# Kernel tuning notes

Hardware: AMD Instinct MI355X
Metric: run time of the kernel (lower is better)

The kernel has to match this reference:

```python
import jax, jax.numpy as jnp
import numpy as np

B, T, DKQ, DV, EKQ, EV, H, OUT = 8, 2048, 64, 64, 128, 128, 4, 32
FF = 4 * EV
NEG = -1e30  # additive mask value (safe stand-in for -inf)


def _ln(x, g, b, eps=1e-5):
    m = x.mean(-1, keepdims=True)
    var = ((x - m) ** 2).mean(-1, keepdims=True)
    return (x - m) * jax.lax.rsqrt(var + eps) * g + b


def _attn(q, k, v, mask):
    # q,k,v: [n, T, E] -> heads [n, H, T, dh]; NOTE: no 1/sqrt(d) scaling (faithful to source)
    n, t, _ = q.shape
    q = q.reshape(n, t, H, -1).transpose(0, 2, 1, 3)
    k = k.reshape(n, t, H, -1).transpose(0, 2, 1, 3)
    v = v.reshape(n, t, H, -1).transpose(0, 2, 1, 3)
    w = jnp.einsum('bhqd,bhkd->bhqk', q, k) + mask  # [n,H,T,T]
    a = jax.nn.softmax(w, axis=-1)
    o = jnp.einsum('bhqk,bhkd->bhqd', a, v)
    return o.transpose(0, 2, 1, 3).reshape(n, t, -1)


def setup_inputs() -> dict:
    key = jax.random.key(0)
    ks = jax.random.split(key, 32)
    w = lambda k, s: jax.random.normal(k, s, jnp.float32) * 0.02
    DIN_A = DKQ + DV
    return {
        'kq': jax.random.normal(ks[0], (B, T, DKQ), jnp.float32),
        'v': jax.random.normal(ks[1], (B, T, DV), jnp.float32),
        # Layer A (input_dim = DKQ+DV, embed = EV)
        'A_Wk': w(ks[2], (DIN_A, EV)), 'A_bk': jnp.zeros((EV,), jnp.float32),
        'A_Wq': w(ks[3], (DIN_A, EV)), 'A_bq': jnp.zeros((EV,), jnp.float32),
        'A_Wv': w(ks[4], (DIN_A, EV)), 'A_bv': jnp.zeros((EV,), jnp.float32),
        'A_f1W': w(ks[5], (EV, FF)), 'A_f1b': jnp.zeros((FF,), jnp.float32),
        'A_f2W': w(ks[6], (FF, EV)), 'A_f2b': jnp.zeros((EV,), jnp.float32),
        'A_n1g': jnp.ones((EV,), jnp.float32), 'A_n1b': jnp.zeros((EV,), jnp.float32),
        'A_n2g': jnp.ones((EV,), jnp.float32), 'A_n2b': jnp.zeros((EV,), jnp.float32),
        # Layer B (kq -> EKQ, vA -> EV)
        'B_Wk': w(ks[7], (DKQ, EKQ)), 'B_bk': jnp.zeros((EKQ,), jnp.float32),
        'B_Wq': w(ks[8], (DKQ, EKQ)), 'B_bq': jnp.zeros((EKQ,), jnp.float32),
        'B_Wv': w(ks[9], (EV, EV)), 'B_bv': jnp.zeros((EV,), jnp.float32),
        'B_f1W': w(ks[10], (EV, FF)), 'B_f1b': jnp.zeros((FF,), jnp.float32),
        'B_f2W': w(ks[11], (FF, EV)), 'B_f2b': jnp.zeros((EV,), jnp.float32),
        # Output head
        'out_W': w(ks[12], (EV, OUT)), 'out_b': jnp.zeros((OUT,), jnp.float32),
    }


def reference(kq, v, A_Wk, A_bk, A_Wq, A_bq, A_Wv, A_bv, A_f1W, A_f1b, A_f2W, A_f2b,
              A_n1g, A_n1b, A_n2g, A_n2b, B_Wk, B_bk, B_Wq, B_bq, B_Wv, B_bv,
              B_f1W, B_f1b, B_f2W, B_f2b, out_W, out_b):
    n, t, _ = kq.shape
    i = jnp.arange(t)[:, None]
    j = jnp.arange(t)[None, :]
    mask_a = jnp.where(j <= i, 0.0, NEG).astype(jnp.float32)               # causal (diag=1)
    mask_b = jnp.where((j < i) | ((i == 0) & (j == 0)), 0.0, NEG).astype(jnp.float32)  # strict causal + (0,0) exception

    # ---- Layer A ----
    X = jnp.concatenate([kq, v], axis=-1)
    K = X @ A_Wk + A_bk
    Q = X @ A_Wq + A_bq
    V = X @ A_Wv + A_bv
    attn_out = _attn(Q, K, V, mask_a)
    h1 = _ln(V + attn_out, A_n1g, A_n1b)
    ff = jax.nn.gelu(h1 @ A_f1W + A_f1b, approximate=False) @ A_f2W + A_f2b
    vA = _ln(h1 + ff, A_n2g, A_n2b)

    # ---- Layer B (no residuals / norms: values is overwritten in source) ----
    K2 = kq @ B_Wk + B_bk
    Q2 = kq @ B_Wq + B_bq
    V2 = vA @ B_Wv + B_bv
    attn_out2 = _attn(Q2, K2, V2, mask_b)
    ff2 = jax.nn.gelu(attn_out2 @ B_f1W + B_f1b, approximate=False) @ B_f2W + B_f2b

    return ff2 @ out_W + out_b
```

## Files before the change

### kernel.cpp

```cpp
#include <hip/hip_runtime.h>
#include <hip/hip_bf16.h>

#define TSEQ 2048
#define NBATCH 8
#define NROWS (NBATCH*TSEQ)
#define EMB 128
#define NH 4
#define DH 32
#define OUTD 32
#define APLANE (NROWS*EMB)

typedef short s8v __attribute__((ext_vector_type(8)));
typedef float f4v __attribute__((ext_vector_type(4)));

__device__ __forceinline__ unsigned short f2bf(float f){
  unsigned int u = __float_as_uint(f);
  unsigned int r = u + 0x7fffu + ((u >> 16) & 1u);
  return (unsigned short)(r >> 16);
}
__device__ __forceinline__ float bf2f(unsigned short u){
  return __uint_as_float(((unsigned int)u) << 16);
}

struct WPack {
  const float* src[10];
  int off[10];
  int ntk[10];
  int rowoff[10];
  int nsh[10];
  int kn[10];
};
__global__ __launch_bounds__(256) void prep_w(WPack p, short* __restrict__ warena){
  int blk = blockIdx.x, m = 0;
  #pragma unroll
  for (int i=0;i<10;i++){
    int nb = p.kn[i] >> 8;
    if (blk < nb){ m = i; break; }
    blk -= nb;
  }
  int idx = blk*256 + threadIdx.x;
  float x = p.src[m][idx];
  int nsh = p.nsh[m];
  int n = idx & ((1<<nsh)-1);
  int k = idx >> nsh;
  int K = p.kn[m] >> nsh;
  unsigned short hi = f2bf(x);
  unsigned short lo = f2bf(x - bf2f(hi));
  short* dh = warena + p.off[m] + (size_t)(p.rowoff[m] + n)*K + k;
  dh[0]        = (short)hi;
  dh[p.ntk[m]] = (short)lo;
}

__global__ __launch_bounds__(256) void xsplit(const float* __restrict__ kq, const float* __restrict__ v,
                                              unsigned short* __restrict__ X){
  int idx = blockIdx.x*256 + threadIdx.x;
  int row = idx >> 7, c = idx & 127;
  float val = (c < 64) ? kq[row*64 + c] : v[row*64 + (c-64)];
  unsigned short hi = f2bf(val);
  X[idx]          = hi;
  X[idx + APLANE] = f2bf(val - bf2f(hi));
}

struct GOuts {
  const float* bias[3];
  float* of[3];
  unsigned short* ob[3];
};
__global__ __launch_bounds__(256) void gemm2(
    const unsigned short* __restrict__ A, int aplane, int lda, int K, int niter,
    const short* __restrict__ wt, int NTK,
    GOuts og, int NT, int nseg, int act){
  __shared__ short As[2][2][64*40];
  const int tid  = threadIdx.x;
  const int w    = tid >> 6;
  const int lane = tid & 63;
  const int col  = lane & 15;
  const int quad = lane >> 4;
  const int row0 = blockIdx.x * 64;
  const int colg = blockIdx.y*64 + w*16 + col;
  const bool two = (aplane != 0);

  f4v acc[4];
  #pragma unroll
  for (int i=0;i<4;i++) acc[i] = (f4v){0.f,0.f,0.f,0.f};

  const int ar = tid >> 2, ac = (tid & 3)*8;
  const unsigned short* abase = A + (size_t)(row0 + ar)*lda;

  s8v pah, pal;
  pah = *(const s8v*)(abase + ac);
  if (two) pal = *(const s8v*)(abase + aplane + ac);

  for (int i=0;i<niter;i++){
    const int buf = i & 1;
    *(s8v*)&As[buf][0][ar*40 + ac] = pah;
    if (two) *(s8v*)&As[buf][1][ar*40 + ac] = pal;
    __syncthreads();
    if (i+1 < niter){
      const int kcol = (i+1)*32 + ac;
      pah = *(const s8v*)(abase + kcol);
      if (two) pal = *(const s8v*)(abase + aplane + kcol);
    }
    const short* wp = wt + (size_t)colg*K + i*32 + quad*8;
    s8v bh = *(const s8v*)wp;
    s8v bl = *(const s8v*)(wp + NTK);
    #pragma unroll
    for (int rt=0;rt<4;rt++){
      s8v ah = *(const s8v*)&As[buf][0][(rt*16 + col)*40 + quad*8];
      acc[rt] = __builtin_amdgcn_mfma_f32_16x16x32_bf16(ah, bh, acc[rt], 0, 0, 0);
      if (two){
        s8v al = *(const s8v*)&As[buf][1][(rt*16 + col)*40 + quad*8];
        acc[rt] = __builtin_amdgcn_mfma_f32_16x16x32_bf16(al, bh, acc[rt], 0, 0, 0);
      }
      acc[rt] = __builtin_amdgcn_mfma_f32_16x16x32_bf16(ah, bl, acc[rt], 0, 0, 0);
    }
  }

  int seg, lcol, ldc;
  if (nseg > 1){ seg = colg >> 7; lcol = colg & 127; ldc = 128; }
  else         { seg = 0; lcol = colg; ldc = NT; }
  const float bv = og.bias[seg][lcol];
  float* of = og.of[seg];
  unsigned short* ob = og.ob[seg];
  #pragma unroll
  for (int rt=0;rt<4;rt++){
    #pragma unroll
    for (int r=0;r<4;r++){
      const int row = row0 + rt*16 + quad*4 + r;
      float val = acc[rt][r] + bv;
      if (act == 1) val = 0.5f*val*(1.f + erff(val*0.70710678118654752440f));
      if (ob) ob[(size_t)row*ldc + lcol] = f2bf(val);
      else    of[(size_t)row*ldc + lcol] = val;
    }
  }
}

__global__ __launch_bounds__(256) void vtrans(const float* __restrict__ V, unsigned short* __restrict__ Vtb){
  __shared__ short Lt[64*40];
  const int tid = threadIdx.x;
  const int t0 = blockIdx.x * 64;
  const int bh = blockIdx.y;
  const int b = bh >> 2, h = bh & 3;
  {
    const int r = tid >> 2, c = (tid & 3)*8;
    const float* src = V + (size_t)(b*TSEQ + t0 + r)*EMB + h*DH + c;
    float4 x0 = *(const float4*)src;
    float4 x1 = *(const float4*)(src + 4);
    s8v kb;
    kb[0]=(short)f2bf(x0.x); kb[1]=(short)f2bf(x0.y); kb[2]=(short)f2bf(x0.z); kb[3]=(short)f2bf(x0.w);
    kb[4]=(short)f2bf(x1.x); kb[5]=(short)f2bf(x1.y); kb[6]=(short)f2bf(x1.z); kb[7]=(short)f2bf(x1.w);
    *(s8v*)&Lt[r*40 + c] = kb;
  }
  __syncthreads();
  const int d = tid >> 3, kc = (tid & 7)*8;
  s8v o;
  #pragma unroll
  for (int j=0;j<8;j++) o[j] = Lt[(kc + j)*40 + d];
  *(s8v*)(Vtb + ((size_t)bh*32 + d)*TSEQ + t0 + kc) = o;
}

#define KT_STRIDE 40
#define VT_STRIDE 72
#define PW_STRIDE 72
__global__ __launch_bounds__(128) void flash3(const unsigned short* __restrict__ Qb,
                                              const unsigned short* __restrict__ Kb,
                                              const unsigned short* __restrict__ Vtb,
                                              float* __restrict__ O0, float* __restrict__ O1,
                                              float* __restrict__ L0, float* __restrict__ L1,
                                              int mode){
  __shared__ short Kt[64*KT_STRIDE];
  __shared__ short Vt[32*VT_STRIDE];
  __shared__ short Pw[2][16*PW_STRIDE];
  const int tid  = threadIdx.x;
  const int w    = tid >> 6;
  const int lane = tid & 63;
  const int col  = lane & 15;
  const int quad = lane >> 4;
  const int bh = blockIdx.y;
  const int b = bh >> 2, h = bh & 3;
  const int par = blockIdx.z;
  float* Op = par ? O1 : O0;
  float* Lp = par ? L1 : L0;
  const int kr = tid >> 1, kc16 = (tid & 1)*16;
  const int vd = tid >> 2, vk16 = (tid & 3)*16;

  for (int pass = 0; pass < 2; pass++){
    const int t = pass ? blockIdx.x : (63 - blockIdx.x);
    const int qbase = t*32 + w*16;
    const int jtmax = t >> 1;

    s8v qf = *(const s8v*)(Qb + (size_t)(b*TSEQ + qbase + col)*EMB + h*DH + quad*8);
    f4v o0 = {0.f,0.f,0.f,0.f}, o1 = {0.f,0.f,0.f,0.f};
    float lr[4] = {0.f,0.f,0.f,0.f};

    if (par <= jtmax){
      s8v ka, kb2, va, vb;
      {
        const unsigned short* kp = Kb + (size_t)(b*TSEQ + par*64 + kr)*EMB + h*DH + kc16;
        ka = *(const s8v*)kp; kb2 = *(const s8v*)(kp + 8);
        const unsigned short* vp = Vtb + ((size_t)bh*32 + vd)*TSEQ + par*64 + vk16;
        va = *(const s8v*)vp; vb = *(const s8v*)(vp + 8);
      }
      for (int jt = par; jt <= jtmax; jt += 2){
        __syncthreads();
        *(s8v*)&Kt[kr*KT_STRIDE + kc16]     = ka;
        *(s8v*)&Kt[kr*KT_STRIDE + kc16 + 8] = kb2;
        *(s8v*)&Vt[vd*VT_STRIDE + vk16]     = va;
        *(s8v*)&Vt[vd*VT_STRIDE + vk16 + 8] = vb;
        __syncthreads();
        if (jt + 2 <= jtmax){
          const unsigned short* kp = Kb + (size_t)(b*TSEQ + (jt+2)*64 + kr)*EMB + h*DH + kc16;
          ka = *(const s8v*)kp; kb2 = *(const s8v*)(kp + 8);
          const unsigned short* vp = Vtb + ((size_t)bh*32 + vd)*TSEQ + (jt+2)*64 + vk16;
          va = *(const s8v*)vp; vb = *(const s8v*)(vp + 8);
        }
        f4v s[4];
        #pragma unroll
        for (int t4=0;t4<4;t4++){
          s8v kf = *(const s8v*)&Kt[(t4*16 + col)*KT_STRIDE + quad*8];
          f4v z = {0.f,0.f,0.f,0.f};
          s[t4] = __builtin_amdgcn_mfma_f32_16x16x32_bf16(qf, kf, z, 0, 0, 0);
        }
        if (jt == jtmax){
          const int j0 = jt*64;
          #pragma unroll
          for (int t4=0;t4<4;t4++){
            const int jg = j0 + t4*16 + col;
            #pragma unroll
            for (int r=0;r<4;r++){
              const int qg = qbase + quad*4 + r;
              const bool ok = (mode==0) ? (jg <= qg) : ((jg < qg) || (qg==0 && jg==0));
              s[t4][r] = ok ? s[t4][r] : -1e30f;
            }
          }
        }
        #pragma unroll
        for (int t4=0;t4<4;t4++){
          #pragma unroll
          for (int r=0;r<4;r++){
            float pv = __expf(s[t4][r]);
            s[t4][r] = pv;
            lr[r] += pv;
            Pw[w][(quad*4+r)*PW_STRIDE + t4*16 + col] = (short)f2bf(pv);
          }
        }
        #pragma unroll
        for (int kk=0;kk<2;kk++){
          s8v pf  = *(const s8v*)&Pw[w][col*PW_STRIDE + kk*32 + quad*8];
          s8v vf0 = *(const s8v*)&Vt[(col)*VT_STRIDE    + kk*32 + quad*8];
          s8v vf1 = *(const s8v*)&Vt[(16+col)*VT_STRIDE + kk*32 + quad*8];
          o0 = __builtin_amdgcn_mfma_f32_16x16x32_bf16(pf, vf0, o0, 0, 0, 0);
          o1 = __builtin_amdgcn_mfma_f32_16x16x32_bf16(pf, vf1, o1, 0, 0, 0);
        }
      }
    }
    float* obase = Op + (size_t)(b*TSEQ + qbase)*EMB + h*DH;
    #pragma unroll
    for (int r=0;r<4;r++){
      float l = lr[r];
      l += __shfl_xor(l,1); l += __shfl_xor(l,2);
      l += __shfl_xor(l,4); l += __shfl_xor(l,8);
      obase[(size_t)(quad*4+r)*EMB + col]      = o0[r];
      obase[(size_t)(quad*4+r)*EMB + 16 + col] = o1[r];
      if (col == 0) Lp[(size_t)(b*TSEQ + qbase + quad*4 + r)*NH + h] = l;
    }
  }
}

__global__ __launch_bounds__(64) void combine_ln(const float* __restrict__ O0, const float* __restrict__ O1,
                                                 const float* __restrict__ L0, const float* __restrict__ L1,
                                                 const float* __restrict__ Vf,
                                                 const float* __restrict__ g, const float* __restrict__ bt,
                                                 unsigned short* __restrict__ outp){
  const int row = blockIdx.x;
  const int tid = threadIdx.x;
  const size_t base = (size_t)row*EMB;
  const int h0 = tid >> 5, h1i = 2 + (tid >> 5);
  const float la = L0[(size_t)row*NH + h0] + L1[(size_t)row*NH + h0];
  const float lb = L0[(size_t)row*NH + h1i] + L1[(size_t)row*NH + h1i];
  float x0 = Vf[base+tid]    + (O0[base+tid]    + O1[base+tid])    / la;
  float x1 = Vf[base+tid+64] + (O0[base+tid+64] + O1[base+tid+64]) / lb;
  float s  = x0 + x1;
  float s2 = x0*x0 + x1*x1;
  #pragma unroll
  for (int off=1; off<64; off<<=1){
    s  += __shfl_xor(s,  off);
    s2 += __shfl_xor(s2, off);
  }
  float mean = s * (1.f/128.f);
  float var  = s2 * (1.f/128.f) - mean*mean;
  float rstd = rsqrtf(var + 1e-5f);
  float y0 = (x0-mean)*rstd*g[tid]    + bt[tid];
  float y1 = (x1-mean)*rstd*g[tid+64] + bt[tid+64];
  unsigned short h0b = f2bf(y0), h1b = f2bf(y1);
  outp[base+tid]             = h0b;
  outp[base+tid+64]          = h1b;
  outp[base+tid+APLANE]      = f2bf(y0 - bf2f(h0b));
  outp[base+tid+64+APLANE]   = f2bf(y1 - bf2f(h1b));
}

__global__ __launch_bounds__(64) void ln2(const unsigned short* __restrict__ Xp, const float* __restrict__ R,
                                          const float* __restrict__ g, const float* __restrict__ bt,
                                          unsigned short* __restrict__ outp){
  const int row = blockIdx.x;
  const int tid = threadIdx.x;
  const size_t base = (size_t)row*EMB;
  float x0 = bf2f(Xp[base+tid])    + bf2f(Xp[base+tid+APLANE])    + R[base+tid];
  float x1 = bf2f(Xp[base+tid+64]) + bf2f(Xp[base+tid+64+APLANE]) + R[base+tid+64];
  float s  = x0 + x1;
  float s2 = x0*x0 + x1*x1;
  #pragma unroll
  for (int off=1; off<64; off<<=1){
    s  += __shfl_xor(s,  off);
    s2 += __shfl_xor(s2, off);
  }
  float mean = s * (1.f/128.f);
  float var  = s2 * (1.f/128.f) - mean*mean;
  float rstd = rsqrtf(var + 1e-5f);
  float y0 = (x0-mean)*rstd*g[tid]    + bt[tid];
  float y1 = (x1-mean)*rstd*g[tid+64] + bt[tid+64];
  unsigned short h0b = f2bf(y0), h1b = f2bf(y1);
  outp[base+tid]             = h0b;
  outp[base+tid+64]          = h1b;
  outp[base+tid+APLANE]      = f2bf(y0 - bf2f(h0b));
  outp[base+tid+64+APLANE]   = f2bf(y1 - bf2f(h1b));
}

__global__ __launch_bounds__(256) void combine_b(const float* __restrict__ O0, const float* __restrict__ O1,
                                                 const float* __restrict__ L0, const float* __restrict__ L1,
                                                 unsigned short* __restrict__ outp){
  const int idx = blockIdx.x*256 + threadIdx.x;
  const int row = idx >> 7, c = idx & 127, h = c >> 5;
  const float l = L0[(size_t)row*NH + h] + L1[(size_t)row*NH + h];
  const float v = (O0[idx] + O1[idx]) / l;
  unsigned short hb = f2bf(v);
  outp[idx]          = hb;
  outp[idx + APLANE] = f2bf(v - bf2f(hb));
}

__global__ __launch_bounds__(256) void out_proj(const float* __restrict__ A,
                                                const float* __restrict__ W, const float* __restrict__ bb,
                                                float* __restrict__ out){
  __shared__ float As[8*128];
  __shared__ float Ws2[128*32];
  const int tid = threadIdx.x;
  const int row0 = blockIdx.x * 8;
  for (int idx = tid; idx < 8*128; idx += 256) As[idx] = A[(size_t)row0*128 + idx];
  for (int idx = tid; idx < 128*32; idx += 256) Ws2[idx] = W[idx];
  __syncthreads();
  const int r = tid >> 5, c = tid & 31;
  float acc = bb[c];
  #pragma unroll 8
  for (int k=0;k<128;k++) acc = fmaf(As[r*128 + k], Ws2[k*32 + c], acc);
  out[(size_t)(row0 + r)*OUTD + c] = acc;
}

extern "C" void kernel_launch(void* const* d_in, const int* in_sizes, int n_in,
                              void* d_out, int out_size, void* d_ws, size_t ws_size,
                              hipStream_t stream) {
  const float* kq    = (const float*)d_in[0];
  const float* v     = (const float*)d_in[1];
  const float* A_Wk  = (const float*)d_in[2];  const float* A_bk  = (const float*)d_in[3];
  const float* A_Wq  = (const float*)d_in[4];  const float* A_bq  = (const float*)d_in[5];
  const float* A_Wv  = (const float*)d_in[6];  const float* A_bv  = (const float*)d_in[7];
  const float* A_f1W = (const float*)d_in[8];  const float* A_f1b = (const float*)d_in[9];
  const float* A_f2W = (const float*)d_in[10]; const float* A_f2b = (const float*)d_in[11];
  const float* A_n1g = (const float*)d_in[12]; const float* A_n1b = (const float*)d_in[13];
  const float* A_n2g = (const float*)d_in[14]; const float* A_n2b = (const float*)d_in[15];
  const float* B_Wk  = (const float*)d_in[16]; const float* B_bk  = (const float*)d_in[17];
  const float* B_Wq  = (const float*)d_in[18]; const float* B_bq  = (const float*)d_in[19];
  const float* B_Wv  = (const float*)d_in[20]; const float* B_bv  = (const float*)d_in[21];
  const float* B_f1W = (const float*)d_in[22]; const float* B_f1b = (const float*)d_in[23];
  const float* B_f2W = (const float*)d_in[24]; const float* B_f2b = (const float*)d_in[25];
  const float* out_W = (const float*)d_in[26]; const float* out_b = (const float*)d_in[27];
  float* out = (float*)d_out;
  (void)in_sizes; (void)n_in; (void)out_size; (void)ws_size;

  char* ws = (char*)d_ws;
  const size_t MB = 1024*1024;
  short* warena = (short*)ws;
  unsigned short* Xs  = (unsigned short*)(ws + 2*MB);
  unsigned short* Qbf = (unsigned short*)(ws + 10*MB);
  unsigned short* Kbf = (unsigned short*)(ws + 14*MB);
  unsigned short* Vtb = (unsigned short*)(ws + 18*MB);
  float* Vf  = (float*)(ws + 22*MB);
  float* O0  = (float*)(ws + 30*MB);
  float* O1  = (float*)(ws + 38*MB);
  float* L0  = (float*)(ws + 46*MB);
  float* L1  = (float*)(ws + 47*MB);
  unsigned short* h1p = (unsigned short*)(ws + 48*MB);
  unsigned short* mid = (unsigned short*)(ws + 56*MB);
  float* ffo = (float*)(ws + 72*MB);
  unsigned short* vAp = (unsigned short*)(ws + 80*MB);

  WPack p;
  const float* srcs[10] = {A_Wq,A_Wk,A_Wv,A_f1W,A_f2W,B_Wq,B_Wk,B_Wv,B_f1W,B_f2W};
  int kn[10]     = {16384,16384,16384,65536,65536,8192,8192,16384,65536,65536};
  int nsh[10]    = {7,7,7,9,7,7,7,7,9,7};
  int off[10]    = {0,0,0,98304,229376,360448,360448,393216,425984,557056};
  int ntk[10]    = {49152,49152,49152,65536,65536,16384,16384,16384,65536,65536};
  int rowoff[10] = {0,128,256,0,0,0,128,0,0,0};
  int nblk = 0;
  for (int i=0;i<10;i++){
    p.src[i]=srcs[i]; p.kn[i]=kn[i]; p.nsh[i]=nsh[i];
    p.off[i]=off[i]; p.ntk[i]=ntk[i]; p.rowoff[i]=rowoff[i];
    nblk += kn[i] >> 8;
  }
  prep_w<<<nblk, 256, 0, stream>>>(p, warena);
  xsplit<<<NROWS*128/256, 256, 0, stream>>>(kq, v, Xs);

  GOuts oQKVA = {{A_bq,A_bk,A_bv},{nullptr,nullptr,Vf},{Qbf,Kbf,nullptr}};
  GOuts oF1A  = {{A_f1b,nullptr,nullptr},{nullptr,nullptr,nullptr},{mid,nullptr,nullptr}};
  GOuts oF2A  = {{A_f2b,nullptr,nullptr},{ffo,nullptr,nullptr},{nullptr,nullptr,nullptr}};
  GOuts oQKB  = {{B_bq,B_bk,nullptr},{nullptr,nullptr,nullptr},{Qbf,Kbf,nullptr}};
  GOuts oVB   = {{B_bv,nullptr,nullptr},{Vf,nullptr,nullptr},{nullptr,nullptr,nullptr}};
  GOuts oF1B  = {{B_f1b,nullptr,nullptr},{nullptr,nullptr,nullptr},{mid,nullptr,nullptr}};
  GOuts oF2B  = {{B_f2b,nullptr,nullptr},{ffo,nullptr,nullptr},{nullptr,nullptr,nullptr}};

  gemm2<<<dim3(256,6), 256, 0, stream>>>(Xs, APLANE, 128, 128, 4, warena + 0,      49152, oQKVA, 384, 3, 0);
  vtrans<<<dim3(32,32), 256, 0, stream>>>(Vf, Vtb);
  flash3<<<dim3(32,32,2), 128, 0, stream>>>(Qbf, Kbf, Vtb, O0, O1, L0, L1, 0);
  combine_ln<<<NROWS, 64, 0, stream>>>(O0, O1, L0, L1, Vf, A_n1g, A_n1b, h1p);
  gemm2<<<dim3(256,8), 256, 0, stream>>>(h1p, APLANE, 128, 128, 4, warena + 98304, 65536, oF1A, 512, 1, 1);
  gemm2<<<dim3(256,2), 256, 0, stream>>>(mid, 0,      512, 512, 16, warena + 229376, 65536, oF2A, 128, 1, 0);
  ln2<<<NROWS, 64, 0, stream>>>(h1p, ffo, A_n2g, A_n2b, vAp);

  gemm2<<<dim3(256,4), 256, 0, stream>>>(Xs, APLANE, 128, 64, 2,  warena + 360448, 16384, oQKB, 256, 2, 0);
  gemm2<<<dim3(256,2), 256, 0, stream>>>(vAp, APLANE, 128, 128, 4, warena + 393216, 16384, oVB, 128, 1, 0);
  vtrans<<<dim3(32,32), 256, 0, stream>>>(Vf, Vtb);
  flash3<<<dim3(32,32,2), 128, 0, stream>>>(Qbf, Kbf, Vtb, O0, O1, L0, L1, 1);
  combine_b<<<NROWS*128/256, 256, 0, stream>>>(O0, O1, L0, L1, h1p);
  gemm2<<<dim3(256,8), 256, 0, stream>>>(h1p, APLANE, 128, 128, 4, warena + 425984, 65536, oF1B, 512, 1, 1);
  gemm2<<<dim3(256,2), 256, 0, stream>>>(mid, 0,      512, 512, 16, warena + 557056, 65536, oF2B, 128, 1, 0);

  out_proj<<<NROWS/8, 256, 0, stream>>>(ffo, out_W, out_b, out);
}
```

Baseline: 310.2 us.

## Fuse V transpose into GEMM epilogue, widen GEMM column tiles, merge prep kernels

```diff
diff --git a/kernel.cpp b/kernel.cpp
--- a/kernel.cpp
+++ b/kernel.cpp
@@ -11,6 +11,7 @@
 #define APLANE (NROWS*EMB)
 
 typedef short s8v __attribute__((ext_vector_type(8)));
+typedef short s4v __attribute__((ext_vector_type(4)));
 typedef float f4v __attribute__((ext_vector_type(4)));
 
 __device__ __forceinline__ unsigned short f2bf(float f){
@@ -30,8 +31,21 @@
   int nsh[10];
   int kn[10];
 };
-__global__ __launch_bounds__(256) void prep_w(WPack p, short* __restrict__ warena){
-  int blk = blockIdx.x, m = 0;
+__global__ __launch_bounds__(256) void prep(WPack p, short* __restrict__ warena,
+                                            const float* __restrict__ kq, const float* __restrict__ v,
+                                            unsigned short* __restrict__ X){
+  int blk = blockIdx.x;
+  if (blk < (NROWS*EMB/256)){
+    int idx = blk*256 + threadIdx.x;
+    int row = idx >> 7, c = idx & 127;
+    float val = (c < 64) ? kq[row*64 + c] : v[row*64 + (c-64)];
+    unsigned short hi = f2bf(val);
+    X[idx]          = hi;
+    X[idx + APLANE] = f2bf(val - bf2f(hi));
+    return;
+  }
+  blk -= (NROWS*EMB/256);
+  int m = 0;
   #pragma unroll
   for (int i=0;i<10;i++){
     int nb = p.kn[i] >> 8;
@@ -51,25 +65,17 @@
   dh[p.ntk[m]] = (short)lo;
 }
 
-__global__ __launch_bounds__(256) void xsplit(const float* __restrict__ kq, const float* __restrict__ v,
-                                              unsigned short* __restrict__ X){
-  int idx = blockIdx.x*256 + threadIdx.x;
-  int row = idx >> 7, c = idx & 127;
-  float val = (c < 64) ? kq[row*64 + c] : v[row*64 + (c-64)];
-  unsigned short hi = f2bf(val);
-  X[idx]          = hi;
-  X[idx + APLANE] = f2bf(val - bf2f(hi));
-}
-
 struct GOuts {
   const float* bias[3];
   float* of[3];
   unsigned short* ob[3];
 };
+template<int CT>
 __global__ __launch_bounds__(256) void gemm2(
     const unsigned short* __restrict__ A, int aplane, int lda, int K, int niter,
     const short* __restrict__ wt, int NTK,
-    GOuts og, int NT, int nseg, int act){
+    GOuts og, int NT, int nseg, int act,
+    unsigned short* __restrict__ vtb, int vcol0){
   __shared__ short As[2][2][64*40];
   const int tid  = threadIdx.x;
   const int w    = tid >> 6;
@@ -77,12 +83,14 @@
   const int col  = lane & 15;
   const int quad = lane >> 4;
   const int row0 = blockIdx.x * 64;
-  const int colg = blockIdx.y*64 + w*16 + col;
+  const int cb   = blockIdx.y*(64*CT) + w*(16*CT) + col;
   const bool two = (aplane != 0);
 
-  f4v acc[4];
-  #pragma unroll
-  for (int i=0;i<4;i++) acc[i] = (f4v){0.f,0.f,0.f,0.f};
+  f4v acc[4][CT];
+  #pragma unroll
+  for (int i=0;i<4;i++)
+    #pragma unroll
+    for (int j=0;j<CT;j++) acc[i][j] = (f4v){0.f,0.f,0.f,0.f};
 
   const int ar = tid >> 2, ac = (tid & 3)*8;
   const unsigned short* abase = A + (size_t)(row0 + ar)*lda;
@@ -90,6 +98,10 @@
   s8v pah, pal;
   pah = *(const s8v*)(abase + ac);
   if (two) pal = *(const s8v*)(abase + aplane + ac);
+
+  const short* wbase[CT];
+  #pragma unroll
+  for (int ct=0;ct<CT;ct++) wbase[ct] = wt + (size_t)(cb + ct*16)*K + quad*8;
 
   for (int i=0;i<niter;i++){
     const int buf = i & 1;
@@ -101,62 +113,73 @@
       pah = *(const s8v*)(abase + kcol);
       if (two) pal = *(const s8v*)(abase + aplane + kcol);
     }
-    const short* wp = wt + (size_t)colg*K + i*32 + quad*8;
-    s8v bh = *(const s8v*)wp;
-    s8v bl = *(const s8v*)(wp + NTK);
+    s8v bh[CT], bl[CT];
+    #pragma unroll
+    for (int ct=0;ct<CT;ct++){
+      bh[ct] = *(const s8v*)(wbase[ct] + i*32);
+      bl[ct] = *(const s8v*)(wbase[ct] + i*32 + NTK);
+    }
     #pragma unroll
     for (int rt=0;rt<4;rt++){
       s8v ah = *(const s8v*)&As[buf][0][(rt*16 + col)*40 + quad*8];
-      acc[rt] = __builtin_amdgcn_mfma_f32_16x16x32_bf16(ah, bh, acc[rt], 0, 0, 0);
+      #pragma unroll
+      for (int ct=0;ct<CT;ct++)
+        acc[rt][ct] = __builtin_amdgcn_mfma_f32_16x16x32_bf16(ah, bh[ct], acc[rt][ct], 0, 0, 0);
       if (two){
         s8v al = *(const s8v*)&As[buf][1][(rt*16 + col)*40 + quad*8];
-        acc[rt] = __builtin_amdgcn_mfma_f32_16x16x32_bf16(al, bh, acc[rt], 0, 0, 0);
+        #pragma unroll
+        for (int ct=0;ct<CT;ct++)
+          acc[rt][ct] = __builtin_amdgcn_mfma_f32_16x16x32_bf16(al, bh[ct], acc[rt][ct], 0, 0, 0);
       }
-      acc[rt] = __builtin_amdgcn_mfma_f32_16x16x32_bf16(ah, bl, acc[rt], 0, 0, 0);
-    }
-  }
-
-  int seg, lcol, ldc;
-  if (nseg > 1){ seg = colg >> 7; lcol = colg & 127; ldc = 128; }
-  else         { seg = 0; lcol = colg; ldc = NT; }
-  const float bv = og.bias[seg][lcol];
-  float* of = og.of[seg];
-  unsigned short* ob = og.ob[seg];
-  #pragma unroll
-  for (int rt=0;rt<4;rt++){
-    #pragma unroll
-    for (int r=0;r<4;r++){
-      const int row = row0 + rt*16 + quad*4 + r;
-      float val = acc[rt][r] + bv;
-      if (act == 1) val = 0.5f*val*(1.f + erff(val*0.70710678118654752440f));
-      if (ob) ob[(size_t)row*ldc + lcol] = f2bf(val);
-      else    of[(size_t)row*ldc + lcol] = val;
-    }
-  }
-}
-
-__global__ __launch_bounds__(256) void vtrans(const float* __restrict__ V, unsigned short* __restrict__ Vtb){
-  __shared__ short Lt[64*40];
-  const int tid = threadIdx.x;
-  const int t0 = blockIdx.x * 64;
-  const int bh = blockIdx.y;
-  const int b = bh >> 2, h = bh & 3;
-  {
-    const int r = tid >> 2, c = (tid & 3)*8;
-    const float* src = V + (size_t)(b*TSEQ + t0 + r)*EMB + h*DH + c;
-    float4 x0 = *(const float4*)src;
-    float4 x1 = *(const float4*)(src + 4);
-    s8v kb;
-    kb[0]=(short)f2bf(x0.x); kb[1]=(short)f2bf(x0.y); kb[2]=(short)f2bf(x0.z); kb[3]=(short)f2bf(x0.w);
-    kb[4]=(short)f2bf(x1.x); kb[5]=(short)f2bf(x1.y); kb[6]=(short)f2bf(x1.z); kb[7]=(short)f2bf(x1.w);
-    *(s8v*)&Lt[r*40 + c] = kb;
-  }
-  __syncthreads();
-  const int d = tid >> 3, kc = (tid & 7)*8;
-  s8v o;
-  #pragma unroll
-  for (int j=0;j<8;j++) o[j] = Lt[(kc + j)*40 + d];
-  *(s8v*)(Vtb + ((size_t)bh*32 + d)*TSEQ + t0 + kc) = o;
+      #pragma unroll
+      for (int ct=0;ct<CT;ct++)
+        acc[rt][ct] = __builtin_amdgcn_mfma_f32_16x16x32_bf16(ah, bl[ct], acc[rt][ct], 0, 0, 0);
+    }
+  }
+
+  const int NB = 64*CT;
+  const int cb0 = (int)blockIdx.y * NB;
+  const bool dotr = (vtb != nullptr) && (cb0 >= vcol0) && (cb0 < vcol0 + 128);
+  short* Lt = &As[0][0][0];
+  if (dotr) __syncthreads();
+
+  #pragma unroll
+  for (int ct=0;ct<CT;ct++){
+    const int cg = cb + ct*16;
+    int seg, lcol, ldc;
+    if (nseg > 1){ seg = cg >> 7; lcol = cg & 127; ldc = 128; }
+    else         { seg = 0; lcol = cg; ldc = NT; }
+    const float bv = og.bias[seg][lcol];
+    float* of = og.of[seg];
+    unsigned short* ob = og.ob[seg];
+    #pragma unroll
+    for (int rt=0;rt<4;rt++){
+      s4v pk;
+      #pragma unroll
+      for (int r=0;r<4;r++){
+        const int row = row0 + rt*16 + quad*4 + r;
+        float val = acc[rt][ct][r] + bv;
+        if (act == 1) val = 0.5f*val*(1.f + erff(val*0.70710678118654752440f));
+        if (ob)      ob[(size_t)row*ldc + lcol] = f2bf(val);
+        else if (of) of[(size_t)row*ldc + lcol] = val;
+        if (dotr) pk[r] = (short)f2bf(val);
+      }
+      if (dotr)
+        *(s4v*)&Lt[(w*(16*CT) + ct*16 + col)*72 + rt*16 + quad*4] = pk;
+    }
+  }
+  if (dotr){
+    __syncthreads();
+    const int b = row0 >> 11, t0 = row0 & 2047;
+    #pragma unroll
+    for (int it=0; it<2*CT; it++){
+      const int cl = it*32 + (tid>>3);
+      const int t8 = (tid&7)*8;
+      s8v o = *(const s8v*)&Lt[cl*72 + t8];
+      const int cr = cb0 + cl - vcol0;
+      *(s8v*)(vtb + ((size_t)((b*4 + (cr>>5))*32 + (cr&31)))*2048 + t0 + t8) = o;
+    }
+  }
 }
 
 #define KT_STRIDE 40
@@ -267,13 +290,13 @@
   }
 }
 
-__global__ __launch_bounds__(64) void combine_ln(const float* __restrict__ O0, const float* __restrict__ O1,
-                                                 const float* __restrict__ L0, const float* __restrict__ L1,
-                                                 const float* __restrict__ Vf,
-                                                 const float* __restrict__ g, const float* __restrict__ bt,
-                                                 unsigned short* __restrict__ outp){
-  const int row = blockIdx.x;
-  const int tid = threadIdx.x;
+__global__ __launch_bounds__(256) void combine_ln(const float* __restrict__ O0, const float* __restrict__ O1,
+                                                  const float* __restrict__ L0, const float* __restrict__ L1,
+                                                  const float* __restrict__ Vf,
+                                                  const float* __restrict__ g, const float* __restrict__ bt,
+                                                  unsigned short* __restrict__ outp){
+  const int row = blockIdx.x*4 + (threadIdx.x >> 6);
+  const int tid = threadIdx.x & 63;
   const size_t base = (size_t)row*EMB;
   const int h0 = tid >> 5, h1i = 2 + (tid >> 5);
   const float la = L0[(size_t)row*NH + h0] + L1[(size_t)row*NH + h0];
@@ -299,11 +322,11 @@
   outp[base+tid+64+APLANE]   = f2bf(y1 - bf2f(h1b));
 }
 
-__global__ __launch_bounds__(64) void ln2(const unsigned short* __restrict__ Xp, const float* __restrict__ R,
-                                          const float* __restrict__ g, const float* __restrict__ bt,
-                                          unsigned short* __restrict__ outp){
-  const int row = blockIdx.x;
-  const int tid = threadIdx.x;
+__global__ __launch_bounds__(256) void ln2(const unsigned short* __restrict__ Xp, const float* __restrict__ R,
+                                           const float* __restrict__ g, const float* __restrict__ bt,
+                                           unsigned short* __restrict__ outp){
+  const int row = blockIdx.x*4 + (threadIdx.x >> 6);
+  const int tid = threadIdx.x & 63;
   const size_t base = (size_t)row*EMB;
   float x0 = bf2f(Xp[base+tid])    + bf2f(Xp[base+tid+APLANE])    + R[base+tid];
   float x1 = bf2f(Xp[base+tid+64]) + bf2f(Xp[base+tid+64+APLANE]) + R[base+tid+64];
@@ -406,32 +429,29 @@
     p.off[i]=off[i]; p.ntk[i]=ntk[i]; p.rowoff[i]=rowoff[i];
     nblk += kn[i] >> 8;
   }
-  prep_w<<<nblk, 256, 0, stream>>>(p, warena);
-  xsplit<<<NROWS*128/256, 256, 0, stream>>>(kq, v, Xs);
+  prep<<<(NROWS*EMB/256) + nblk, 256, 0, stream>>>(p, warena, kq, v, Xs);
 
   GOuts oQKVA = {{A_bq,A_bk,A_bv},{nullptr,nullptr,Vf},{Qbf,Kbf,nullptr}};
   GOuts oF1A  = {{A_f1b,nullptr,nullptr},{nullptr,nullptr,nullptr},{mid,nullptr,nullptr}};
   GOuts oF2A  = {{A_f2b,nullptr,nullptr},{ffo,nullptr,nullptr},{nullptr,nullptr,nullptr}};
   GOuts oQKB  = {{B_bq,B_bk,nullptr},{nullptr,nullptr,nullptr},{Qbf,Kbf,nullptr}};
-  GOuts oVB   = {{B_bv,nullptr,nullptr},{Vf,nullptr,nullptr},{nullptr,nullptr,nullptr}};
+  GOuts oVB   = {{B_bv,nullptr,nullptr},{nullptr,nullptr,nullptr},{nullptr,nullptr,nullptr}};
   GOuts oF1B  = {{B_f1b,nullptr,nullptr},{nullptr,nullptr,nullptr},{mid,nullptr,nullptr}};
   GOuts oF2B  = {{B_f2b,nullptr,nullptr},{ffo,nullptr,nullptr},{nullptr,nullptr,nullptr}};
 
-  gemm2<<<dim3(256,6), 256, 0, stream>>>(Xs, APLANE, 128, 128, 4, warena + 0,      49152, oQKVA, 384, 3, 0);
-  vtrans<<<dim3(32,32), 256, 0, stream>>>(Vf, Vtb);
+  gemm2<2><<<dim3(256,3), 256, 0, stream>>>(Xs, APLANE, 128, 128, 4, warena + 0,      49152, oQKVA, 384, 3, 0, Vtb, 256);
   flash3<<<dim3(32,32,2), 128, 0, stream>>>(Qbf, Kbf, Vtb, O0, O1, L0, L1, 0);
-  combine_ln<<<NROWS, 64, 0, stream>>>(O0, O1, L0, L1, Vf, A_n1g, A_n1b, h1p);
-  gemm2<<<dim3(256,8), 256, 0, stream>>>(h1p, APLANE, 128, 128, 4, warena + 98304, 65536, oF1A, 512, 1, 1);
-  gemm2<<<dim3(256,2), 256, 0, stream>>>(mid, 0,      512, 512, 16, warena + 229376, 65536, oF2A, 128, 1, 0);
-  ln2<<<NROWS, 64, 0, stream>>>(h1p, ffo, A_n2g, A_n2b, vAp);
-
-  gemm2<<<dim3(256,4), 256, 0, stream>>>(Xs, APLANE, 128, 64, 2,  warena + 360448, 16384, oQKB, 256, 2, 0);
-  gemm2<<<dim3(256,2), 256, 0, stream>>>(vAp, APLANE, 128, 128, 4, warena + 393216, 16384, oVB, 128, 1, 0);
-  vtrans<<<dim3(32,32), 256, 0, stream>>>(Vf, Vtb);
+  combine_ln<<<NROWS/4, 256, 0, stream>>>(O0, O1, L0, L1, Vf, A_n1g, A_n1b, h1p);
+  gemm2<2><<<dim3(256,4), 256, 0, stream>>>(h1p, APLANE, 128, 128, 4, warena + 98304, 65536, oF1A, 512, 1, 1, nullptr, 0);
+  gemm2<1><<<dim3(256,2), 256, 0, stream>>>(mid, 0,      512, 512, 16, warena + 229376, 65536, oF2A, 128, 1, 0, nullptr, 0);
+  ln2<<<NROWS/4, 256, 0, stream>>>(h1p, ffo, A_n2g, A_n2b, vAp);
+
+  gemm2<2><<<dim3(256,2), 256, 0, stream>>>(Xs, APLANE, 128, 64, 2,  warena + 360448, 16384, oQKB, 256, 2, 0, nullptr, 0);
+  gemm2<1><<<dim3(256,2), 256, 0, stream>>>(vAp, APLANE, 128, 128, 4, warena + 393216, 16384, oVB, 128, 1, 0, Vtb, 0);
   flash3<<<dim3(32,32,2), 128, 0, stream>>>(Qbf, Kbf, Vtb, O0, O1, L0, L1, 1);
   combine_b<<<NROWS*128/256, 256, 0, stream>>>(O0, O1, L0, L1, h1p);
-  gemm2<<<dim3(256,8), 256, 0, stream>>>(h1p, APLANE, 128, 128, 4, warena + 425984, 65536, oF1B, 512, 1, 1);
-  gemm2<<<dim3(256,2), 256, 0, stream>>>(mid, 0,      512, 512, 16, warena + 557056, 65536, oF2B, 128, 1, 0);
+  gemm2<2><<<dim3(256,4), 256, 0, stream>>>(h1p, APLANE, 128, 128, 4, warena + 425984, 65536, oF1B, 512, 1, 1, nullptr, 0);
+  gemm2<1><<<dim3(256,2), 256, 0, stream>>>(mid, 0,      512, 512, 16, warena + 557056, 65536, oF2B, 128, 1, 0, nullptr, 0);
 
   out_proj<<<NROWS/8, 256, 0, stream>>>(ffo, out_W, out_b, out);
 }
```

Result: no change. 314.5 us (+1.4%).
